# Kernel optimization log

Measured on AMD Instinct MI355X. Metric: run time of the kernel, lower is better.

## Reference

```python
import jax, jax.numpy as jnp
import numpy as np

D_MODEL = 256
D_INNER = 512   # expand * d_model
NHEADS = 8
HEADDIM = 64    # d_inner // nheads
NGROUPS = 1
MDIST = 16


def setup_inputs() -> dict:
    key = jax.random.key(0)
    ks = jax.random.split(key, 12)
    B, L, Q = 4, 2048, 300
    in_key = jax.random.normal(ks[0], (B, L, D_MODEL), jnp.float32)
    in_query = jax.random.normal(ks[1], (B, Q, D_MODEL), jnp.float32)
    dist = jax.random.normal(ks[2], (B, L, Q, MDIST), jnp.float32)

    def lin(k, out_f, in_f):  # torch nn.Linear default init (kaiming-uniform-ish)
        bound = 1.0 / np.sqrt(in_f)
        return jax.random.uniform(k, (out_f, in_f), jnp.float32, -bound, bound)

    W_key = lin(ks[3], 2 * D_INNER + 2 * NGROUPS + NHEADS, D_MODEL)
    W_query = lin(ks[4], D_INNER, D_MODEL)
    W_bc = lin(ks[5], 2 * NGROUPS, MDIST)
    W_dt = lin(ks[6], NHEADS, MDIST)
    # dt_bias init (inverse-softplus of dt sampled log-uniform in [1e-4, 0.1])
    dt_min, dt_max = 1e-4, 0.1
    dtv = jnp.exp(jax.random.uniform(ks[7], (NHEADS,)) * (np.log(dt_max) - np.log(dt_min)) + np.log(dt_min))
    dtv = jnp.clip(dtv, 1e-4, None)
    dt_bias = dtv + jnp.log(-jnp.expm1(-dtv))
    A_log = jnp.log(jax.random.uniform(ks[8], (NHEADS,), minval=1.0, maxval=16.0))
    Dp = jnp.ones((NHEADS,), jnp.float32)
    W_out_key = lin(ks[9], D_MODEL, D_INNER)
    W_out_query = lin(ks[10], D_MODEL, D_INNER)
    key_norm_w = jnp.ones((D_INNER,), jnp.float32)
    ln_w = jnp.ones((D_INNER,), jnp.float32)
    ln_b = jnp.zeros((D_INNER,), jnp.float32)
    return dict(in_key=in_key, in_query=in_query, dist=dist, W_key=W_key, W_query=W_query,
                W_bc=W_bc, W_dt=W_dt, dt_bias=dt_bias, A_log=A_log, Dp=Dp,
                W_out_key=W_out_key, W_out_query=W_out_query, key_norm_w=key_norm_w,
                ln_w=ln_w, ln_b=ln_b)


def _issm_scan(x, S0, dt, A, Bm, Cm, Dp):
    """Selective scan with per-(l,h,n) dt and per-(l,n) B,C (ngroups=1).
    x: (B,L,H,P)  dt: (B,L,H,N)  Bm,Cm: (B,L,N)  S0: (B,H,P,N)  A: (H,)  Dp: (H,)
    """
    xs = (jnp.moveaxis(x, 1, 0), jnp.moveaxis(dt, 1, 0),
          jnp.moveaxis(Bm, 1, 0), jnp.moveaxis(Cm, 1, 0))

    def step(S, inp):
        xl, dtl, Bl, Cl = inp               # (B,H,P), (B,H,N), (B,N), (B,N)
        dA = jnp.exp(dtl * A[None, :, None])            # (B,H,N)
        dBx = (dtl * Bl[:, None, :])[:, :, None, :] * xl[:, :, :, None]
        S = S * dA[:, :, None, :] + dBx                 # (B,H,P,N)
        y = jnp.einsum('bhpn,bn->bhp', S, Cl) + Dp[None, :, None] * xl
        return S, y

    Sf, ys = jax.lax.scan(step, S0, xs)
    return jnp.moveaxis(ys, 0, 1), Sf       # (B,L,H,P), (B,H,P,N)


def reference(in_key, in_query, dist, W_key, W_query, W_bc, W_dt, dt_bias, A_log, Dp,
              W_out_key, W_out_query, key_norm_w, ln_w, ln_b):
    B, L, _ = in_key.shape
    Q = in_query.shape[1]
    zxbcdt = in_key @ W_key.T                            # (B,L,2*Din+2g+H)
    z = zxbcdt[..., :D_INNER]
    x = zxbcdt[..., D_INNER:2 * D_INNER].reshape(B, L, NHEADS, HEADDIM)
    b_bias = zxbcdt[..., 2 * D_INNER:2 * D_INNER + 1]    # (B,L,1)
    c_bias = zxbcdt[..., 2 * D_INNER + 1:2 * D_INNER + 2]
    dt_proj_bias = zxbcdt[..., 2 * D_INNER + 2:]         # (B,L,H)

    # initial state: (B,H,P,Q) -- state dim N == num_queries
    S0 = (in_query @ W_query.T).reshape(B, Q, NHEADS, HEADDIM).transpose(0, 2, 3, 1)
    A = -jnp.exp(A_log)                                  # (H,), constant over state dim

    bc = jnp.einsum('blqm,cm->blqc', dist, W_bc)         # (B,L,Q,2)
    Bm = bc[..., 0] + b_bias                             # (B,L,Q)
    Cm = bc[..., 1] + c_bias
    dtb = jnp.einsum('blqm,hm->blhq', dist, W_dt)        # (B,L,H,Q)
    dt = jax.nn.softplus(dtb + dt_proj_bias[..., None] + dt_bias[None, None, :, None])

    y_f, S_f = _issm_scan(x, S0, dt, A, Bm, Cm, Dp)
    # bidirectional: backward branch uses identical (cloned) x/B/C, flipped along L
    y_b, S_b = _issm_scan(x[:, ::-1], S0, dt[:, ::-1], A, Bm[:, ::-1], Cm[:, ::-1], Dp)
    y = (y_f + y_b[:, ::-1]) * 0.5
    S = (S_f + S_b) * 0.5

    key = y.reshape(B, L, D_INNER)
    g = key * jax.nn.silu(z)                             # gated RMSNorm, norm_before_gate=False
    key = g * jax.lax.rsqrt(jnp.mean(g * g, -1, keepdims=True) + 1e-5) * key_norm_w
    out_key = key @ W_out_key.T

    ls = S.transpose(0, 3, 1, 2).reshape(B, Q, D_INNER)  # b h p q -> b q (h p)
    mu = jnp.mean(ls, -1, keepdims=True)
    var = jnp.mean((ls - mu) ** 2, -1, keepdims=True)
    ls = (ls - mu) * jax.lax.rsqrt(var + 1e-5) * ln_w + ln_b
    out_query = ls @ W_out_query.T
    return out_key, out_query
```

## Files before the change

### kernel.cpp

```cpp
#include <hip/hip_runtime.h>
#include <hip/hip_bf16.h>

#define D_MODEL 256
#define D_INNER 512
#define NHEADS 8
#define HEADDIM 64
#define MDIST 16
#define BB 4
#define LL 2048
#define QQ 300
#define QP 320
#define NSEG 16
#define SEGLEN 128

typedef unsigned short ushort_t;
typedef __attribute__((ext_vector_type(8))) short bf16x8;
typedef __attribute__((ext_vector_type(4))) float f32x4;
typedef __attribute__((ext_vector_type(2))) float f32x2;

__device__ __forceinline__ void bf16_split(float v, ushort_t& hi, ushort_t& lo) {
    __hip_bfloat16 h = __float2bfloat16(v);
    float hf = __bfloat162float(h);
    __hip_bfloat16 l = __float2bfloat16(v - hf);
    hi = *(ushort_t*)&h;
    lo = *(ushort_t*)&l;
}

__device__ __forceinline__ f32x2 shfl_xor2(f32x2 v, int m) {
    f32x2 r;
    r.x = __shfl_xor(v.x, m, 64);
    r.y = __shfl_xor(v.y, m, 64);
    return r;
}

__global__ __launch_bounds__(256) void c_split(const float* __restrict__ in,
                                               ushort_t* __restrict__ hi,
                                               ushort_t* __restrict__ lo, int n) {
    int i = blockIdx.x * 256 + threadIdx.x;
    if (i >= n) return;
    ushort_t h, l;
    bf16_split(in[i], h, l);
    hi[i] = h;
    lo[i] = l;
}

__global__ __launch_bounds__(256) void gemm_bf16s(const ushort_t* __restrict__ Ah,
                                                  const ushort_t* __restrict__ Al,
                                                  const ushort_t* __restrict__ Bh,
                                                  const ushort_t* __restrict__ Bl,
                                                  float* __restrict__ C,
                                                  int M, int N, int K) {
    int w = threadIdx.x >> 6, lane = threadIdx.x & 63;
    int n0 = blockIdx.x * 64;
    int m0 = blockIdx.y * 128 + w * 32;
    int lm = lane & 15, lk = (lane >> 4) * 8;
    f32x4 acc[2][4];
#pragma unroll
    for (int i = 0; i < 2; i++)
#pragma unroll
        for (int j = 0; j < 4; j++) acc[i][j] = {0.f, 0.f, 0.f, 0.f};

    for (int k0 = 0; k0 < K; k0 += 32) {
        bf16x8 ah[2], al[2], bh[4], blo[4];
#pragma unroll
        for (int mf = 0; mf < 2; mf++) {
            int row = m0 + mf * 16 + lm;
            if (row >= M) row = M - 1;
            size_t off = (size_t)row * K + k0 + lk;
            ah[mf] = *(const bf16x8*)(Ah + off);
            al[mf] = *(const bf16x8*)(Al + off);
        }
#pragma unroll
        for (int nf = 0; nf < 4; nf++) {
            int col = n0 + nf * 16 + lm;
            size_t off = (size_t)col * K + k0 + lk;
            bh[nf]  = *(const bf16x8*)(Bh + off);
            blo[nf] = *(const bf16x8*)(Bl + off);
        }
#pragma unroll
        for (int mf = 0; mf < 2; mf++)
#pragma unroll
            for (int nf = 0; nf < 4; nf++) {
                acc[mf][nf] = __builtin_amdgcn_mfma_f32_16x16x32_bf16(ah[mf], bh[nf],  acc[mf][nf], 0, 0, 0);
                acc[mf][nf] = __builtin_amdgcn_mfma_f32_16x16x32_bf16(ah[mf], blo[nf], acc[mf][nf], 0, 0, 0);
                acc[mf][nf] = __builtin_amdgcn_mfma_f32_16x16x32_bf16(al[mf], bh[nf],  acc[mf][nf], 0, 0, 0);
            }
    }
#pragma unroll
    for (int mf = 0; mf < 2; mf++)
#pragma unroll
        for (int nf = 0; nf < 4; nf++)
#pragma unroll
            for (int r = 0; r < 4; r++) {
                int m = m0 + mf * 16 + (lane >> 4) * 4 + r;
                if (m < M) C[(size_t)m * N + n0 + nf * 16 + lm] = acc[mf][nf][r];
            }
}

__global__ __launch_bounds__(256) void k1b_bias(const float* __restrict__ in_key,
                                                const float* __restrict__ W_key,
                                                float* __restrict__ bias10) {
    int w = threadIdx.x >> 6, lane = threadIdx.x & 63;
    int row = blockIdx.x * 4 + w;
    float4 a = *(const float4*)(in_key + (size_t)row * 256 + lane * 4);
#pragma unroll
    for (int c = 0; c < 10; c++) {
        float4 b = *(const float4*)(W_key + (size_t)(1024 + c) * 256 + lane * 4);
        float t = a.x * b.x + a.y * b.y + a.z * b.z + a.w * b.w;
#pragma unroll
        for (int o = 32; o > 0; o >>= 1) t += __shfl_down(t, o, 64);
        if (lane == 0) bias10[row * 10 + c] = t;
    }
}

__global__ __launch_bounds__(256) void k2_dist(const float* __restrict__ dist,
                                               const float* __restrict__ bias10,
                                               const float* __restrict__ W_bc,
                                               const float* __restrict__ W_dt,
                                               const float* __restrict__ dt_bias,
                                               const float* __restrict__ A_log,
                                               float* __restrict__ dA,
                                               float* __restrict__ dtB,
                                               float* __restrict__ Cm) {
    __shared__ float sWbc[32], sWdt[128], sb[8], sA[8];
    int tid = threadIdx.x;
    if (tid < 32) sWbc[tid] = W_bc[tid];
    else if (tid < 160) sWdt[tid - 32] = W_dt[tid - 32];
    else if (tid < 168) sb[tid - 160] = dt_bias[tid - 160];
    else if (tid < 176) sA[tid - 168] = -expf(A_log[tid - 168]);
    __syncthreads();
    int gid = blockIdx.x * 256 + tid;
    if (gid >= BB * LL * QQ) return;
    int q = gid % QQ;
    int bl = gid / QQ;
    const float* dp = dist + (size_t)gid * 16;
    float d[16];
    float4 d0 = *(const float4*)(dp + 0);
    float4 d1 = *(const float4*)(dp + 4);
    float4 d2 = *(const float4*)(dp + 8);
    float4 d3 = *(const float4*)(dp + 12);
    d[0]=d0.x; d[1]=d0.y; d[2]=d0.z; d[3]=d0.w;
    d[4]=d1.x; d[5]=d1.y; d[6]=d1.z; d[7]=d1.w;
    d[8]=d2.x; d[9]=d2.y; d[10]=d2.z; d[11]=d2.w;
    d[12]=d3.x; d[13]=d3.y; d[14]=d3.z; d[15]=d3.w;
    float bc0 = 0.f, bc1 = 0.f;
#pragma unroll
    for (int m = 0; m < 16; m++) {
        bc0 = fmaf(d[m], sWbc[m], bc0);
        bc1 = fmaf(d[m], sWbc[16 + m], bc1);
    }
    float Bmv = bc0 + bias10[bl * 10 + 0];
    float Cv  = bc1 + bias10[bl * 10 + 1];
    Cm[bl * QP + q] = Cv;
#pragma unroll
    for (int h = 0; h < 8; h++) {
        float t = 0.f;
#pragma unroll
        for (int m = 0; m < 16; m++) t = fmaf(d[m], sWdt[h * 16 + m], t);
        float pre = t + bias10[bl * 10 + 2 + h] + sb[h];
        float dt = (pre > 20.f) ? pre : log1pf(expf(pre));
        int o = (bl * 8 + h) * QP + q;
        dA[o]  = expf(sA[h] * dt);
        dtB[o] = dt * Bmv;
    }
}

__global__ __launch_bounds__(256) void k2b_segdecay(const float* __restrict__ dA,
                                                    float* __restrict__ segd) {
    int gid = blockIdx.x * 256 + threadIdx.x;
    if (gid >= BB * NSEG * 8 * QP) return;
    int q = gid % QP; int r = gid / QP;
    int h = r % 8; r /= 8;
    int s = r % NSEG; int b = r / NSEG;
    int base = ((b * LL + s * SEGLEN) * 8 + h) * QP + q;
    float p = 1.f;
    for (int i = 0; i < SEGLEN; i++) p *= dA[base + i * 8 * QP];
    segd[gid] = p;
}

__global__ __launch_bounds__(512) void pass_ac(const float* __restrict__ dA,
                                               const float* __restrict__ dtB,
                                               const float* __restrict__ Cm,
                                               const float* __restrict__ zx,
                                               float* __restrict__ S_local,
                                               float* __restrict__ yf,
                                               float* __restrict__ yb) {
    __shared__ __align__(16) float sOp[2][4096];
    int seg = blockIdx.x, bh = blockIdx.y, dir = blockIdx.z;
    int tid = threadIdx.x;
    int w = tid >> 6, lane = tid & 63;
    int b = bh >> 3, h = bh & 7;
    f32x2 S2[20];
#pragma unroll
    for (int j = 0; j < 20; j++) S2[j] = {0.f, 0.f};
    float* __restrict__ yo = dir ? yb : yf;

    auto stage = [&](int g, int buf) {
#pragma unroll
        for (int rep = 0; rep < 2; rep++) {
            int flat = tid + rep * 512;
            int it = flat >> 8;
            int pos = (flat & 255) * 4;
            int i = g * 4 + it;
            int l = dir ? (LL - 1 - (seg * SEGLEN + i)) : (seg * SEGLEN + i);
            int bl = b * LL + l;
            const float* src;
            if (pos < 320)      src = dA  + (size_t)(bl * 8 + h) * QP + pos;
            else if (pos < 640) src = dtB + (size_t)(bl * 8 + h) * QP + (pos - 320);
            else if (pos < 960) src = Cm + (size_t)bl * QP + (pos - 640);
            else                src = zx + (size_t)bl * 1024 + 512 + h * 64 + (pos - 960);
            *(float4*)&sOp[buf][it * 1024 + pos] = *(const float4*)src;
        }
    };
    stage(0, 0);
    const int NGRP = SEGLEN / 4;
    for (int g = 0; g < NGRP; g++) {
        __syncthreads();
        if (g + 1 < NGRP) stage(g + 1, (g + 1) & 1);
        const float* bufg = &sOp[g & 1][0];
#pragma unroll
        for (int it = 0; it < 4; it++) {
            const float* Bq = bufg + it * 1024;
            float4 xA = *(const float4*)(Bq + 960 + 8 * w);
            float4 xB = *(const float4*)(Bq + 964 + 8 * w);
            f32x2 x2[4] = {{xA.x, xA.y}, {xA.z, xA.w}, {xB.x, xB.y}, {xB.z, xB.w}};
            f32x2 y0 = {0.f, 0.f}, y1 = {0.f, 0.f}, y2v = {0.f, 0.f}, y3 = {0.f, 0.f};
#pragma unroll
            for (int k = 0; k < 5; k++) {
                int idx = k * 64 + lane;
                float a  = Bq[idx];
                float bb = Bq[320 + idx];
                float c  = Bq[640 + idx];
                f32x2 a2 = {a, a}, b2 = {bb, bb}, c2 = {c, c};
                f32x2 s;
                s = S2[k * 4 + 0] * a2 + b2 * x2[0]; S2[k * 4 + 0] = s; y0  += s * c2;
                s = S2[k * 4 + 1] * a2 + b2 * x2[1]; S2[k * 4 + 1] = s; y1  += s * c2;
                s = S2[k * 4 + 2] * a2 + b2 * x2[2]; S2[k * 4 + 2] = s; y2v += s * c2;
                s = S2[k * 4 + 3] * a2 + b2 * x2[3]; S2[k * 4 + 3] = s; y3  += s * c2;
            }
            f32x2 g0 = (lane & 1) ? y0 : y1;
            f32x2 g1 = (lane & 1) ? y2v : y3;
            g0 = shfl_xor2(g0, 1);
            g1 = shfl_xor2(g1, 1);
            f32x2 k0 = ((lane & 1) ? y1 : y0) + g0;
            f32x2 k1 = ((lane & 1) ? y3 : y2v) + g1;
            f32x2 gg = (lane & 2) ? k0 : k1;
            gg = shfl_xor2(gg, 2);
            f32x2 z = ((lane & 2) ? k1 : k0) + gg;
            z += shfl_xor2(z, 4);
            z += shfl_xor2(z, 8);
            z += shfl_xor2(z, 16);
            z += shfl_xor2(z, 32);
            if (lane < 4) {
                int i = g * 4 + it;
                int l = dir ? (LL - 1 - (seg * SEGLEN + i)) : (seg * SEGLEN + i);
                int bl = b * LL + l;
                *(f32x2*)(yo + (size_t)(bl * 8 + h) * 64 + 8 * w + 2 * lane) = z;
            }
        }
    }
    size_t base = (size_t)((dir * NSEG + seg) * 32 + bh) * QP * 64;
#pragma unroll
    for (int k = 0; k < 5; k++) {
        int n = k * 64 + lane;
        float4 v0 = {S2[k * 4 + 0].x, S2[k * 4 + 0].y, S2[k * 4 + 1].x, S2[k * 4 + 1].y};
        float4 v1 = {S2[k * 4 + 2].x, S2[k * 4 + 2].y, S2[k * 4 + 3].x, S2[k * 4 + 3].y};
        *(float4*)&S_local[base + (size_t)n * 64 + 8 * w] = v0;
        *(float4*)&S_local[base + (size_t)n * 64 + 8 * w + 4] = v1;
    }
}

__global__ __launch_bounds__(256) void pass_b(const float* __restrict__ S_local,
                                              const float* __restrict__ segd,
                                              const float* __restrict__ S0q,
                                              float* __restrict__ S_in,
                                              float* __restrict__ Savg) {
    int gid = blockIdx.x * 256 + threadIdx.x;
    if (gid >= BB * 8 * QP * 64) return;
    int p = gid & 63; int r = gid >> 6;
    int n = r % QP; r /= QP;
    int h = r & 7; int b = r >> 3;
    int bh = b * 8 + h;
    float s0 = (n < QQ) ? S0q[(size_t)(b * QQ + n) * 512 + h * 64 + p] : 0.f;
    float Sf = 0.f, Sb = 0.f;
    for (int dir = 0; dir < 2; dir++) {
        float S = s0;
        for (int s = 0; s < NSEG; s++) {
            size_t idx = (size_t)(((dir * NSEG + s) * 32 + bh) * QP + n) * 64 + p;
            S_in[idx] = S;
            int sf = dir ? (NSEG - 1 - s) : s;
            float dec = segd[((b * NSEG + sf) * 8 + h) * QP + n];
            S = fmaf(S, dec, S_local[idx]);
        }
        if (dir == 0) Sf = S; else Sb = S;
    }
    Savg[((bh) * QP + n) * 64 + p] = 0.5f * (Sf + Sb);
}

__global__ __launch_bounds__(256) void k3_corr(const float* __restrict__ dA,
                                               const float* __restrict__ Cm,
                                               const float* __restrict__ Sin,
                                               float* __restrict__ yf,
                                               float* __restrict__ yb) {
    __shared__ __align__(16) ushort_t sAh[128][48], sAl[128][48];
    __shared__ __align__(16) ushort_t sBh[64][48], sBl[64][48];
    __shared__ float pref[8][32];
    int seg = blockIdx.x, bh = blockIdx.y, dir = blockIdx.z;
    int b = bh >> 3, h = bh & 7;
    int tid = threadIdx.x;
    int w = tid >> 6, lane = tid & 63;
    int lm = lane & 15, lkq = lane >> 4;
    f32x4 acc[2][4];
#pragma unroll
    for (int i = 0; i < 2; i++)
#pragma unroll
        for (int j = 0; j < 4; j++) acc[i][j] = {0.f, 0.f, 0.f, 0.f};
    size_t sinBase = (size_t)((dir * NSEG + seg) * 32 + bh) * QP * 64;
    int nl = tid & 31, iseg = tid >> 5;

    for (int k0 = 0; k0 < QP; k0 += 32) {
        __syncthreads();
#pragma unroll
        for (int r = 0; r < 8; r++) {
            int flat = tid + r * 256;
            int kn = flat >> 6, p = flat & 63;
            float v = Sin[sinBase + (size_t)(k0 + kn) * 64 + p];
            ushort_t hi, lo;
            bf16_split(v, hi, lo);
            sBh[p][kn] = hi;
            sBl[p][kn] = lo;
        }
        float da[16], cm[16];
#pragma unroll
        for (int k = 0; k < 16; k++) {
            int i = iseg * 16 + k;
            int l = dir ? (LL - 1 - (seg * SEGLEN + i)) : (seg * SEGLEN + i);
            int bl = b * LL + l;
            da[k] = dA[(size_t)(bl * 8 + h) * QP + k0 + nl];
            cm[k] = Cm[(size_t)bl * QP + k0 + nl];
        }
        float lp = 1.f;
#pragma unroll
        for (int k = 0; k < 16; k++) lp *= da[k];
        pref[iseg][nl] = lp;
        __syncthreads();
        if (tid < 32) {
            float c = 1.f;
#pragma unroll
            for (int s = 0; s < 8; s++) {
                float t = pref[s][tid];
                pref[s][tid] = c;
                c *= t;
            }
        }
        __syncthreads();
        float cum = pref[iseg][nl];
#pragma unroll
        for (int k = 0; k < 16; k++) {
            cum *= da[k];
            float v = cum * cm[k];
            ushort_t hi, lo;
            bf16_split(v, hi, lo);
            int i = iseg * 16 + k;
            sAh[i][nl] = hi;
            sAl[i][nl] = lo;
        }
        __syncthreads();
        bf16x8 ah[2], al[2], bhf[4], blf[4];
#pragma unroll
        for (int mf = 0; mf < 2; mf++) {
            int row = w * 32 + mf * 16 + lm;
            ah[mf] = *(const bf16x8*)&sAh[row][lkq * 8];
            al[mf] = *(const bf16x8*)&sAl[row][lkq * 8];
        }
#pragma unroll
        for (int nf = 0; nf < 4; nf++) {
            int p = nf * 16 + lm;
            bhf[nf] = *(const bf16x8*)&sBh[p][lkq * 8];
            blf[nf] = *(const bf16x8*)&sBl[p][lkq * 8];
        }
#pragma unroll
        for (int mf = 0; mf < 2; mf++)
#pragma unroll
            for (int nf = 0; nf < 4; nf++) {
                acc[mf][nf] = __builtin_amdgcn_mfma_f32_16x16x32_bf16(ah[mf], bhf[nf], acc[mf][nf], 0, 0, 0);
                acc[mf][nf] = __builtin_amdgcn_mfma_f32_16x16x32_bf16(ah[mf], blf[nf], acc[mf][nf], 0, 0, 0);
                acc[mf][nf] = __builtin_amdgcn_mfma_f32_16x16x32_bf16(al[mf], bhf[nf], acc[mf][nf], 0, 0, 0);
            }
    }
    float* __restrict__ yo = dir ? yb : yf;
#pragma unroll
    for (int mf = 0; mf < 2; mf++)
#pragma unroll
        for (int nf = 0; nf < 4; nf++)
#pragma unroll
            for (int r = 0; r < 4; r++) {
                int i = w * 32 + mf * 16 + lkq * 4 + r;
                int p = nf * 16 + lm;
                int l = dir ? (LL - 1 - (seg * SEGLEN + i)) : (seg * SEGLEN + i);
                size_t idx = (size_t)((b * LL + l) * 8 + h) * 64 + p;
                yo[idx] += acc[mf][nf][r];
            }
}

__global__ __launch_bounds__(512) void k4_gate(const float* __restrict__ yf,
                                               const float* __restrict__ yb,
                                               const float* __restrict__ zx,
                                               const float* __restrict__ Dp,
                                               const float* __restrict__ knw,
                                               ushort_t* __restrict__ kh,
                                               ushort_t* __restrict__ kl) {
    int bl = blockIdx.x;
    int t = threadIdx.x;
    int h = t >> 6;
    float x = zx[(size_t)bl * 1024 + 512 + t];
    float yv = 0.5f * (yf[(size_t)bl * 512 + t] + yb[(size_t)bl * 512 + t]) + Dp[h] * x;
    float z = zx[(size_t)bl * 1024 + t];
    float g = yv * (z / (1.f + expf(-z)));
    float v = g * g;
#pragma unroll
    for (int o = 32; o > 0; o >>= 1) v += __shfl_down(v, o, 64);
    __shared__ float rs[8];
    __shared__ float stot;
    if ((t & 63) == 0) rs[t >> 6] = v;
    __syncthreads();
    if (t == 0) {
        float s = 0.f;
#pragma unroll
        for (int i = 0; i < 8; i++) s += rs[i];
        stot = s;
    }
    __syncthreads();
    float rms = rsqrtf(stot / 512.f + 1e-5f);
    float kv = g * rms * knw[t];
    ushort_t hi, lo;
    bf16_split(kv, hi, lo);
    kh[(size_t)bl * 512 + t] = hi;
    kl[(size_t)bl * 512 + t] = lo;
}

__global__ __launch_bounds__(512) void k5_ln(const float* __restrict__ Savg,
                                             const float* __restrict__ lnw,
                                             const float* __restrict__ lnb,
                                             ushort_t* __restrict__ lh,
                                             ushort_t* __restrict__ ll) {
    int bq = blockIdx.x;
    int b = bq / QQ, q = bq % QQ;
    int t = threadIdx.x;
    int h = t >> 6, p = t & 63;
    float v = Savg[((b * 8 + h) * QP + q) * 64 + p];
    float s1 = v, s2 = v * v;
#pragma unroll
    for (int o = 32; o > 0; o >>= 1) {
        s1 += __shfl_down(s1, o, 64);
        s2 += __shfl_down(s2, o, 64);
    }
    __shared__ float r1[8], r2[8];
    __shared__ float smu, srv;
    if ((t & 63) == 0) { r1[t >> 6] = s1; r2[t >> 6] = s2; }
    __syncthreads();
    if (t == 0) {
        float a = 0.f, c = 0.f;
#pragma unroll
        for (int i = 0; i < 8; i++) { a += r1[i]; c += r2[i]; }
        float mu = a / 512.f;
        float var = c / 512.f - mu * mu;
        smu = mu;
        srv = rsqrtf(var + 1e-5f);
    }
    __syncthreads();
    float ov = (v - smu) * srv * lnw[t] + lnb[t];
    ushort_t hi, lo;
    bf16_split(ov, hi, lo);
    lh[(size_t)bq * 512 + t] = hi;
    ll[(size_t)bq * 512 + t] = lo;
}

extern "C" void kernel_launch(void* const* d_in, const int* in_sizes, int n_in,
                              void* d_out, int out_size, void* d_ws, size_t ws_size,
                              hipStream_t stream) {
    const float* in_key    = (const float*)d_in[0];
    const float* in_query  = (const float*)d_in[1];
    const float* dist      = (const float*)d_in[2];
    const float* W_key     = (const float*)d_in[3];
    const float* W_query   = (const float*)d_in[4];
    const float* W_bc      = (const float*)d_in[5];
    const float* W_dt      = (const float*)d_in[6];
    const float* dt_bias   = (const float*)d_in[7];
    const float* A_log     = (const float*)d_in[8];
    const float* Dp        = (const float*)d_in[9];
    const float* W_out_key = (const float*)d_in[10];
    const float* W_out_query = (const float*)d_in[11];
    const float* key_norm_w = (const float*)d_in[12];
    const float* ln_w      = (const float*)d_in[13];
    const float* ln_b      = (const float*)d_in[14];

    float* out_key = (float*)d_out;
    float* out_query = out_key + (size_t)BB * LL * D_MODEL;

    char* w8 = (char*)d_ws;
    auto alloc = [&](size_t bytes) {
        char* ptr = w8;
        w8 += (bytes + 255) & ~(size_t)255;
        return ptr;
    };
    float* zx     = (float*)alloc((size_t)8192 * 1024 * 4);
    float* bias10 = (float*)alloc((size_t)8192 * 10 * 4);
    float* S0q    = (float*)alloc((size_t)1200 * 512 * 4);
    float* dAb    = (float*)alloc((size_t)8192 * 8 * QP * 4);
    float* dtBb   = (float*)alloc((size_t)8192 * 8 * QP * 4);
    float* Cmb    = (float*)alloc((size_t)8192 * QP * 4);
    float* segd   = (float*)alloc((size_t)BB * NSEG * 8 * QP * 4);
    float* Sloc   = (float*)alloc((size_t)2 * NSEG * 32 * QP * 64 * 4);
    float* Sin    = (float*)alloc((size_t)2 * NSEG * 32 * QP * 64 * 4);
    float* yfb    = (float*)alloc((size_t)8192 * 512 * 4);
    float* ybb    = (float*)alloc((size_t)8192 * 512 * 4);
    float* Savg   = (float*)alloc((size_t)32 * QP * 64 * 4);
    ushort_t* ink_h  = (ushort_t*)alloc((size_t)2097152 * 2);
    ushort_t* ink_l  = (ushort_t*)alloc((size_t)2097152 * 2);
    ushort_t* wk_h   = (ushort_t*)alloc((size_t)262144 * 2);
    ushort_t* wk_l   = (ushort_t*)alloc((size_t)262144 * 2);
    ushort_t* inq_h  = (ushort_t*)alloc((size_t)307200 * 2);
    ushort_t* inq_l  = (ushort_t*)alloc((size_t)307200 * 2);
    ushort_t* wq_h   = (ushort_t*)alloc((size_t)131072 * 2);
    ushort_t* wq_l   = (ushort_t*)alloc((size_t)131072 * 2);
    ushort_t* keyb_h = (ushort_t*)alloc((size_t)4194304 * 2);
    ushort_t* keyb_l = (ushort_t*)alloc((size_t)4194304 * 2);
    ushort_t* wok_h  = (ushort_t*)alloc((size_t)131072 * 2);
    ushort_t* wok_l  = (ushort_t*)alloc((size_t)131072 * 2);
    ushort_t* lsn_h  = (ushort_t*)alloc((size_t)614400 * 2);
    ushort_t* lsn_l  = (ushort_t*)alloc((size_t)614400 * 2);
    ushort_t* woq_h  = (ushort_t*)alloc((size_t)131072 * 2);
    ushort_t* woq_l  = (ushort_t*)alloc((size_t)131072 * 2);

    c_split<<<8192, 256, 0, stream>>>(in_key, ink_h, ink_l, 2097152);
    c_split<<<1024, 256, 0, stream>>>(W_key, wk_h, wk_l, 262144);
    c_split<<<1200, 256, 0, stream>>>(in_query, inq_h, inq_l, 307200);
    c_split<<<512, 256, 0, stream>>>(W_query, wq_h, wq_l, 131072);
    c_split<<<512, 256, 0, stream>>>(W_out_key, wok_h, wok_l, 131072);
    c_split<<<512, 256, 0, stream>>>(W_out_query, woq_h, woq_l, 131072);

    gemm_bf16s<<<dim3(16, 64), 256, 0, stream>>>(ink_h, ink_l, wk_h, wk_l, zx, 8192, 1024, 256);
    k1b_bias<<<2048, 256, 0, stream>>>(in_key, W_key, bias10);
    gemm_bf16s<<<dim3(8, 10), 256, 0, stream>>>(inq_h, inq_l, wq_h, wq_l, S0q, 1200, 512, 256);

    k2_dist<<<9600, 256, 0, stream>>>(dist, bias10, W_bc, W_dt, dt_bias, A_log, dAb, dtBb, Cmb);
    k2b_segdecay<<<640, 256, 0, stream>>>(dAb, segd);

    pass_ac<<<dim3(NSEG, 32, 2), 512, 0, stream>>>(dAb, dtBb, Cmb, zx, Sloc, yfb, ybb);
    pass_b<<<2560, 256, 0, stream>>>(Sloc, segd, S0q, Sin, Savg);
    k3_corr<<<dim3(NSEG, 32, 2), 256, 0, stream>>>(dAb, Cmb, Sin, yfb, ybb);

    k4_gate<<<8192, 512, 0, stream>>>(yfb, ybb, zx, Dp, key_norm_w, keyb_h, keyb_l);
    gemm_bf16s<<<dim3(4, 64), 256, 0, stream>>>(keyb_h, keyb_l, wok_h, wok_l, out_key, 8192, 256, 512);

    k5_ln<<<1200, 512, 0, stream>>>(Savg, ln_w, ln_b, lsn_h, lsn_l);
    gemm_bf16s<<<dim3(4, 10), 256, 0, stream>>>(lsn_h, lsn_l, woq_h, woq_l, out_query, 1200, 256, 512);
}
```

Measured before the change: 901.3 us.

## Interleave dA/dtB buffers and give each scan thread 16 head-dim columns

The dA and dt*B intermediates are now written interleaved as float2 pairs, so the scan kernel stages them with one contiguous load. pass_ac drops to 256 threads per block, with each thread holding 16 p-columns of state (80 float2 registers) instead of 8. The cross-lane y reduction is rewritten with DPP and ds_swizzle in place of shuffles. The aim is more work per thread and cheaper reductions, at the cost of much higher register pressure and lower occupancy; k2b_segdecay and k3_corr now read dA with a stride-2 pattern.

```diff
diff --git a/kernel.cpp b/kernel.cpp
--- a/kernel.cpp
+++ b/kernel.cpp
@@ -33,6 +33,21 @@
     return r;
 }
 
+template<int CTRL>
+__device__ __forceinline__ f32x2 dpp2(f32x2 v) {
+    f32x2 r;
+    r.x = __int_as_float(__builtin_amdgcn_update_dpp(0, __float_as_int(v.x), CTRL, 0xF, 0xF, true));
+    r.y = __int_as_float(__builtin_amdgcn_update_dpp(0, __float_as_int(v.y), CTRL, 0xF, 0xF, true));
+    return r;
+}
+template<int OFF>
+__device__ __forceinline__ f32x2 swz2(f32x2 v) {
+    f32x2 r;
+    r.x = __int_as_float(__builtin_amdgcn_ds_swizzle(__float_as_int(v.x), OFF));
+    r.y = __int_as_float(__builtin_amdgcn_ds_swizzle(__float_as_int(v.y), OFF));
+    return r;
+}
+
 __global__ __launch_bounds__(256) void c_split(const float* __restrict__ in,
                                                ushort_t* __restrict__ hi,
                                                ushort_t* __restrict__ lo, int n) {
@@ -119,8 +134,7 @@
                                                const float* __restrict__ W_dt,
                                                const float* __restrict__ dt_bias,
                                                const float* __restrict__ A_log,
-                                               float* __restrict__ dA,
-                                               float* __restrict__ dtB,
+                                               float* __restrict__ dAB,
                                                float* __restrict__ Cm) {
     __shared__ float sWbc[32], sWdt[128], sb[8], sA[8];
     int tid = threadIdx.x;
@@ -160,26 +174,27 @@
         float pre = t + bias10[bl * 10 + 2 + h] + sb[h];
         float dt = (pre > 20.f) ? pre : log1pf(expf(pre));
         int o = (bl * 8 + h) * QP + q;
-        dA[o]  = expf(sA[h] * dt);
-        dtB[o] = dt * Bmv;
-    }
-}
-
-__global__ __launch_bounds__(256) void k2b_segdecay(const float* __restrict__ dA,
+        float2 v;
+        v.x = expf(sA[h] * dt);
+        v.y = dt * Bmv;
+        *(float2*)(dAB + (size_t)o * 2) = v;
+    }
+}
+
+__global__ __launch_bounds__(256) void k2b_segdecay(const float* __restrict__ dAB,
                                                     float* __restrict__ segd) {
     int gid = blockIdx.x * 256 + threadIdx.x;
     if (gid >= BB * NSEG * 8 * QP) return;
     int q = gid % QP; int r = gid / QP;
     int h = r % 8; r /= 8;
     int s = r % NSEG; int b = r / NSEG;
-    int base = ((b * LL + s * SEGLEN) * 8 + h) * QP + q;
+    size_t base = (size_t)((b * LL + s * SEGLEN) * 8 + h) * QP + q;
     float p = 1.f;
-    for (int i = 0; i < SEGLEN; i++) p *= dA[base + i * 8 * QP];
+    for (int i = 0; i < SEGLEN; i++) p *= dAB[(base + (size_t)i * 8 * QP) * 2];
     segd[gid] = p;
 }
 
-__global__ __launch_bounds__(512) void pass_ac(const float* __restrict__ dA,
-                                               const float* __restrict__ dtB,
+__global__ __launch_bounds__(256) void pass_ac(const float* __restrict__ dAB,
                                                const float* __restrict__ Cm,
                                                const float* __restrict__ zx,
                                                float* __restrict__ S_local,
@@ -189,27 +204,26 @@
     int seg = blockIdx.x, bh = blockIdx.y, dir = blockIdx.z;
     int tid = threadIdx.x;
     int w = tid >> 6, lane = tid & 63;
+    int p0 = w * 16;
     int b = bh >> 3, h = bh & 7;
-    f32x2 S2[20];
-#pragma unroll
-    for (int j = 0; j < 20; j++) S2[j] = {0.f, 0.f};
+    f32x2 S2[40];
+#pragma unroll
+    for (int j = 0; j < 40; j++) S2[j] = {0.f, 0.f};
     float* __restrict__ yo = dir ? yb : yf;
-
+    bool s1 = (lane & 1) != 0, s2b = (lane & 2) != 0, s4 = (lane & 4) != 0;
+
+    int pos = tid * 4;
     auto stage = [&](int g, int buf) {
 #pragma unroll
-        for (int rep = 0; rep < 2; rep++) {
-            int flat = tid + rep * 512;
-            int it = flat >> 8;
-            int pos = (flat & 255) * 4;
-            int i = g * 4 + it;
+        for (int r = 0; r < 4; r++) {
+            int i = g * 4 + r;
             int l = dir ? (LL - 1 - (seg * SEGLEN + i)) : (seg * SEGLEN + i);
             int bl = b * LL + l;
             const float* src;
-            if (pos < 320)      src = dA  + (size_t)(bl * 8 + h) * QP + pos;
-            else if (pos < 640) src = dtB + (size_t)(bl * 8 + h) * QP + (pos - 320);
+            if (pos < 640)      src = dAB + (size_t)(bl * 8 + h) * 640 + pos;
             else if (pos < 960) src = Cm + (size_t)bl * QP + (pos - 640);
             else                src = zx + (size_t)bl * 1024 + 512 + h * 64 + (pos - 960);
-            *(float4*)&sOp[buf][it * 1024 + pos] = *(const float4*)src;
+            *(float4*)&sOp[buf][r * 1024 + pos] = *(const float4*)src;
         }
     };
     stage(0, 0);
@@ -221,41 +235,44 @@
 #pragma unroll
         for (int it = 0; it < 4; it++) {
             const float* Bq = bufg + it * 1024;
-            float4 xA = *(const float4*)(Bq + 960 + 8 * w);
-            float4 xB = *(const float4*)(Bq + 964 + 8 * w);
-            f32x2 x2[4] = {{xA.x, xA.y}, {xA.z, xA.w}, {xB.x, xB.y}, {xB.z, xB.w}};
-            f32x2 y0 = {0.f, 0.f}, y1 = {0.f, 0.f}, y2v = {0.f, 0.f}, y3 = {0.f, 0.f};
+            float4 xq0 = *(const float4*)(Bq + 960 + p0);
+            float4 xq1 = *(const float4*)(Bq + 964 + p0);
+            float4 xq2 = *(const float4*)(Bq + 968 + p0);
+            float4 xq3 = *(const float4*)(Bq + 972 + p0);
+            f32x2 x2[8] = {{xq0.x, xq0.y}, {xq0.z, xq0.w}, {xq1.x, xq1.y}, {xq1.z, xq1.w},
+                           {xq2.x, xq2.y}, {xq2.z, xq2.w}, {xq3.x, xq3.y}, {xq3.z, xq3.w}};
+            f32x2 y[8];
+#pragma unroll
+            for (int j = 0; j < 8; j++) y[j] = {0.f, 0.f};
 #pragma unroll
             for (int k = 0; k < 5; k++) {
-                int idx = k * 64 + lane;
-                float a  = Bq[idx];
-                float bb = Bq[320 + idx];
-                float c  = Bq[640 + idx];
-                f32x2 a2 = {a, a}, b2 = {bb, bb}, c2 = {c, c};
-                f32x2 s;
-                s = S2[k * 4 + 0] * a2 + b2 * x2[0]; S2[k * 4 + 0] = s; y0  += s * c2;
-                s = S2[k * 4 + 1] * a2 + b2 * x2[1]; S2[k * 4 + 1] = s; y1  += s * c2;
-                s = S2[k * 4 + 2] * a2 + b2 * x2[2]; S2[k * 4 + 2] = s; y2v += s * c2;
-                s = S2[k * 4 + 3] * a2 + b2 * x2[3]; S2[k * 4 + 3] = s; y3  += s * c2;
-            }
-            f32x2 g0 = (lane & 1) ? y0 : y1;
-            f32x2 g1 = (lane & 1) ? y2v : y3;
-            g0 = shfl_xor2(g0, 1);
-            g1 = shfl_xor2(g1, 1);
-            f32x2 k0 = ((lane & 1) ? y1 : y0) + g0;
-            f32x2 k1 = ((lane & 1) ? y3 : y2v) + g1;
-            f32x2 gg = (lane & 2) ? k0 : k1;
-            gg = shfl_xor2(gg, 2);
-            f32x2 z = ((lane & 2) ? k1 : k0) + gg;
-            z += shfl_xor2(z, 4);
-            z += shfl_xor2(z, 8);
-            z += shfl_xor2(z, 16);
-            z += shfl_xor2(z, 32);
-            if (lane < 4) {
+                int n = k * 64 + lane;
+                f32x2 ab = *(const f32x2*)(Bq + 2 * n);
+                float c = Bq[640 + n];
+                f32x2 a2 = {ab.x, ab.x}, b2 = {ab.y, ab.y}, c2 = {c, c};
+#pragma unroll
+                for (int j = 0; j < 8; j++) {
+                    f32x2 s = S2[k * 8 + j] * a2 + b2 * x2[j];
+                    S2[k * 8 + j] = s;
+                    y[j] += s * c2;
+                }
+            }
+            f32x2 u, v, z0, z1, z2, z3, w0, w1, q;
+            u = s1 ? y[1] : y[0]; v = s1 ? y[0] : y[1]; z0 = u + dpp2<0xB1>(v);
+            u = s1 ? y[3] : y[2]; v = s1 ? y[2] : y[3]; z1 = u + dpp2<0xB1>(v);
+            u = s1 ? y[5] : y[4]; v = s1 ? y[4] : y[5]; z2 = u + dpp2<0xB1>(v);
+            u = s1 ? y[7] : y[6]; v = s1 ? y[6] : y[7]; z3 = u + dpp2<0xB1>(v);
+            u = s2b ? z1 : z0; v = s2b ? z0 : z1; w0 = u + dpp2<0x4E>(v);
+            u = s2b ? z3 : z2; v = s2b ? z2 : z3; w1 = u + dpp2<0x4E>(v);
+            u = s4 ? w1 : w0; v = s4 ? w0 : w1; q = u + swz2<0x101F>(v);
+            q = q + dpp2<0x128>(q);
+            q = q + swz2<0x401F>(q);
+            q = q + shfl_xor2(q, 32);
+            if (lane < 8) {
                 int i = g * 4 + it;
                 int l = dir ? (LL - 1 - (seg * SEGLEN + i)) : (seg * SEGLEN + i);
                 int bl = b * LL + l;
-                *(f32x2*)(yo + (size_t)(bl * 8 + h) * 64 + 8 * w + 2 * lane) = z;
+                *(f32x2*)(yo + (size_t)(bl * 8 + h) * 64 + p0 + 2 * lane) = q;
             }
         }
     }
@@ -263,10 +280,12 @@
 #pragma unroll
     for (int k = 0; k < 5; k++) {
         int n = k * 64 + lane;
-        float4 v0 = {S2[k * 4 + 0].x, S2[k * 4 + 0].y, S2[k * 4 + 1].x, S2[k * 4 + 1].y};
-        float4 v1 = {S2[k * 4 + 2].x, S2[k * 4 + 2].y, S2[k * 4 + 3].x, S2[k * 4 + 3].y};
-        *(float4*)&S_local[base + (size_t)n * 64 + 8 * w] = v0;
-        *(float4*)&S_local[base + (size_t)n * 64 + 8 * w + 4] = v1;
+#pragma unroll
+        for (int t = 0; t < 4; t++) {
+            float4 vv = {S2[k * 8 + 2 * t].x, S2[k * 8 + 2 * t].y,
+                         S2[k * 8 + 2 * t + 1].x, S2[k * 8 + 2 * t + 1].y};
+            *(float4*)&S_local[base + (size_t)n * 64 + p0 + 4 * t] = vv;
+        }
     }
 }
 
@@ -297,7 +316,7 @@
     Savg[((bh) * QP + n) * 64 + p] = 0.5f * (Sf + Sb);
 }
 
-__global__ __launch_bounds__(256) void k3_corr(const float* __restrict__ dA,
+__global__ __launch_bounds__(256) void k3_corr(const float* __restrict__ dAB,
                                                const float* __restrict__ Cm,
                                                const float* __restrict__ Sin,
                                                float* __restrict__ yf,
@@ -336,7 +355,7 @@
             int i = iseg * 16 + k;
             int l = dir ? (LL - 1 - (seg * SEGLEN + i)) : (seg * SEGLEN + i);
             int bl = b * LL + l;
-            da[k] = dA[(size_t)(bl * 8 + h) * QP + k0 + nl];
+            da[k] = dAB[((size_t)(bl * 8 + h) * QP + k0 + nl) * 2];
             cm[k] = Cm[(size_t)bl * QP + k0 + nl];
         }
         float lp = 1.f;
@@ -507,8 +526,7 @@
     float* zx     = (float*)alloc((size_t)8192 * 1024 * 4);
     float* bias10 = (float*)alloc((size_t)8192 * 10 * 4);
     float* S0q    = (float*)alloc((size_t)1200 * 512 * 4);
-    float* dAb    = (float*)alloc((size_t)8192 * 8 * QP * 4);
-    float* dtBb   = (float*)alloc((size_t)8192 * 8 * QP * 4);
+    float* dABb   = (float*)alloc((size_t)8192 * 8 * QP * 2 * 4);
     float* Cmb    = (float*)alloc((size_t)8192 * QP * 4);
     float* segd   = (float*)alloc((size_t)BB * NSEG * 8 * QP * 4);
     float* Sloc   = (float*)alloc((size_t)2 * NSEG * 32 * QP * 64 * 4);
@@ -544,12 +562,12 @@
     k1b_bias<<<2048, 256, 0, stream>>>(in_key, W_key, bias10);
     gemm_bf16s<<<dim3(8, 10), 256, 0, stream>>>(inq_h, inq_l, wq_h, wq_l, S0q, 1200, 512, 256);
 
-    k2_dist<<<9600, 256, 0, stream>>>(dist, bias10, W_bc, W_dt, dt_bias, A_log, dAb, dtBb, Cmb);
-    k2b_segdecay<<<640, 256, 0, stream>>>(dAb, segd);
-
-    pass_ac<<<dim3(NSEG, 32, 2), 512, 0, stream>>>(dAb, dtBb, Cmb, zx, Sloc, yfb, ybb);
+    k2_dist<<<9600, 256, 0, stream>>>(dist, bias10, W_bc, W_dt, dt_bias, A_log, dABb, Cmb);
+    k2b_segdecay<<<640, 256, 0, stream>>>(dABb, segd);
+
+    pass_ac<<<dim3(NSEG, 32, 2), 256, 0, stream>>>(dABb, Cmb, zx, Sloc, yfb, ybb);
     pass_b<<<2560, 256, 0, stream>>>(Sloc, segd, S0q, Sin, Savg);
-    k3_corr<<<dim3(NSEG, 32, 2), 256, 0, stream>>>(dAb, Cmb, Sin, yfb, ybb);
+    k3_corr<<<dim3(NSEG, 32, 2), 256, 0, stream>>>(dABb, Cmb, Sin, yfb, ybb);
 
     k4_gate<<<8192, 512, 0, stream>>>(yfb, ybb, zx, Dp, key_norm_w, keyb_h, keyb_l);
     gemm_bf16s<<<dim3(4, 64), 256, 0, stream>>>(keyb_h, keyb_l, wok_h, wok_l, out_key, 8192, 256, 512);
```

Measured after the change: 907.5 us. About the same (+0.7%).
